# Kernel optimization log

Hardware: AMD Instinct MI355X
Metric: run time of the kernel (lower is better)

The kernel has to match this reference:

```python
import jax, jax.numpy as jnp
import numpy as np

ANCHORS = jnp.array([[10,14],[23,27],[37,58],[81,82],[135,169],[344,319]], jnp.float32)
ANCHOR_MASK = [[3,4,5],[1,2,3]]
NUM_CLASSES = 80
IMAGE_HW = (1080.0, 1920.0)   # (h, w) of source image
MAX_BOXES = 20
SCORE_THR = 0.6
IOU_THR = 0.5
NEG = jnp.float32(-1e30)      # sentinel for suppressed scores


def decode_layer(feats, anchors_l):
    """yolo_head + yolo_correct_boxes for one detection head. feats: [1,H,W,3*(C+5)]."""
    _, H, W, _ = feats.shape
    f = feats.reshape(H, W, 3, NUM_CLASSES + 5)
    gy, gx = jnp.meshgrid(jnp.arange(H), jnp.arange(W), indexing='ij')
    grid = jnp.stack([gx, gy], axis=-1).astype(f.dtype)[:, :, None, :]  # [H,W,1,2] (x,y)
    input_hw = jnp.array([H * 32.0, W * 32.0], f.dtype)                 # network input (h,w)
    # decode
    box_xy = (jax.nn.sigmoid(f[..., :2]) + grid) / jnp.array([W, H], f.dtype)
    box_wh = jnp.exp(f[..., 2:4]) * anchors_l / input_hw[::-1]          # anchors_l: [3,2] (w,h)
    conf = jax.nn.sigmoid(f[..., 4:5])
    probs = jax.nn.sigmoid(f[..., 5:])
    # letterbox correction (yolo_correct_boxes)
    box_yx = box_xy[..., ::-1]
    box_hw = box_wh[..., ::-1]
    image_hw = jnp.array(IMAGE_HW, f.dtype)
    new_shape = jnp.round(image_hw * jnp.min(input_hw / image_hw))
    offset = (input_hw - new_shape) / 2.0 / input_hw
    scale = input_hw / new_shape
    box_yx = (box_yx - offset) * scale
    box_hw = box_hw * scale
    mins = box_yx - box_hw / 2.0
    maxes = box_yx + box_hw / 2.0
    boxes = jnp.concatenate([mins, maxes], axis=-1) * jnp.concatenate([image_hw, image_hw])
    return boxes.reshape(-1, 4), (conf * probs).reshape(-1, NUM_CLASSES)


def nms_per_class(boxes, scores_c):
    """Greedy NMS for one class. boxes: [N,4] (ymin,xmin,ymax,xmax), scores_c: [N].
    Fixed-size (jit-friendly) equivalent of boolean_mask + tf.image.non_max_suppression:
    below-threshold scores are masked to NEG; output is padded to MAX_BOXES slots."""
    areas = (boxes[:, 2] - boxes[:, 0]) * (boxes[:, 3] - boxes[:, 1])
    s0 = jnp.where(scores_c >= SCORE_THR, scores_c, NEG)

    def body(s, _):
        i = jnp.argmax(s)
        valid = s[i] > NEG / 2
        b = boxes[i]
        yx1 = jnp.maximum(b[:2], boxes[:, :2])
        yx2 = jnp.minimum(b[2:], boxes[:, 2:])
        inter = jnp.prod(jnp.clip(yx2 - yx1, 0.0), axis=-1)
        union = areas[i] + areas - inter
        iou = jnp.where(union > 0, inter / union, 0.0)
        s_next = jnp.where((iou > IOU_THR) & valid, NEG, s)
        s_next = s_next.at[i].set(NEG)
        return s_next, (i, valid)

    _, (idx, valid) = jax.lax.scan(body, s0, None, length=MAX_BOXES)
    sel_boxes = boxes[idx] * valid[:, None].astype(boxes.dtype)   # [MAX_BOXES,4]
    sel_scores = scores_c[idx] * valid.astype(scores_c.dtype)     # [MAX_BOXES]
    return sel_boxes, sel_scores, valid


def setup_inputs() -> dict:
    key = jax.random.key(0)
    k0, k1 = jax.random.split(key)
    feats0 = jax.random.normal(k0, (1, 96, 96, 3 * (NUM_CLASSES + 5)), jnp.float32)
    feats1 = jax.random.normal(k1, (1, 192, 192, 3 * (NUM_CLASSES + 5)), jnp.float32)
    return {"feats0": feats0, "feats1": feats1}


def reference(feats0, feats1):
    b0, s0 = decode_layer(feats0, ANCHORS[jnp.array(ANCHOR_MASK[0])])
    b1, s1 = decode_layer(feats1, ANCHORS[jnp.array(ANCHOR_MASK[1])])
    boxes = jnp.concatenate([b0, b1], axis=0)      # [N,4]
    scores = jnp.concatenate([s0, s1], axis=0)     # [N,80]
    sel_b, sel_s, valid = jax.vmap(nms_per_class, in_axes=(None, 1))(boxes, scores)
    classes = jnp.broadcast_to(jnp.arange(NUM_CLASSES, dtype=jnp.int32)[:, None],
                               (NUM_CLASSES, MAX_BOXES))
    classes = jnp.where(valid, classes, -1).reshape(-1)
    return sel_b.reshape(-1, 4), sel_s.reshape(-1), classes
```

## Files before the change

kernel.cpp:

```cpp
#include <hip/hip_runtime.h>

#define NCLS 80
#define MAXB 20
#define N0 27648
#define N1 110592
#define NTOT (N0 + N1)
#define CAP 8192
#define DT 512
#define DSTAGE 3072
#define CNT_STRIDE 16
#define NMS_T 1024
#define NB 256
#define TARGET 128
#define SCAP 256

__device__ __forceinline__ float sigf(float x) {
    return 1.0f / (1.0f + expf(-x));
}

__device__ __forceinline__ unsigned wave_max_bcast(unsigned x) {
    unsigned t;
    t = (unsigned)__builtin_amdgcn_update_dpp((int)x, (int)x, 0x111, 0xF, 0xF, false); x = x > t ? x : t;
    t = (unsigned)__builtin_amdgcn_update_dpp((int)x, (int)x, 0x112, 0xF, 0xF, false); x = x > t ? x : t;
    t = (unsigned)__builtin_amdgcn_update_dpp((int)x, (int)x, 0x114, 0xF, 0xF, false); x = x > t ? x : t;
    t = (unsigned)__builtin_amdgcn_update_dpp((int)x, (int)x, 0x118, 0xF, 0xF, false); x = x > t ? x : t;
    t = (unsigned)__builtin_amdgcn_update_dpp((int)x, (int)x, 0x142, 0xF, 0xF, false); x = x > t ? x : t;
    t = (unsigned)__builtin_amdgcn_update_dpp((int)x, (int)x, 0x143, 0xF, 0xF, false); x = x > t ? x : t;
    return (unsigned)__builtin_amdgcn_readlane((int)x, 63);
}

__device__ __forceinline__ unsigned wave_min_bcast(unsigned x) {
    unsigned t;
    t = (unsigned)__builtin_amdgcn_update_dpp((int)x, (int)x, 0x111, 0xF, 0xF, false); x = x < t ? x : t;
    t = (unsigned)__builtin_amdgcn_update_dpp((int)x, (int)x, 0x112, 0xF, 0xF, false); x = x < t ? x : t;
    t = (unsigned)__builtin_amdgcn_update_dpp((int)x, (int)x, 0x114, 0xF, 0xF, false); x = x < t ? x : t;
    t = (unsigned)__builtin_amdgcn_update_dpp((int)x, (int)x, 0x118, 0xF, 0xF, false); x = x < t ? x : t;
    t = (unsigned)__builtin_amdgcn_update_dpp((int)x, (int)x, 0x142, 0xF, 0xF, false); x = x < t ? x : t;
    t = (unsigned)__builtin_amdgcn_update_dpp((int)x, (int)x, 0x143, 0xF, 0xF, false); x = x < t ? x : t;
    return (unsigned)__builtin_amdgcn_readlane((int)x, 63);
}

__device__ __forceinline__ unsigned wave_incl_scan(unsigned x) {
    x += (unsigned)__builtin_amdgcn_update_dpp(0, (int)x, 0x111, 0xF, 0xF, false);
    x += (unsigned)__builtin_amdgcn_update_dpp(0, (int)x, 0x112, 0xF, 0xF, false);
    x += (unsigned)__builtin_amdgcn_update_dpp(0, (int)x, 0x114, 0xF, 0xF, false);
    x += (unsigned)__builtin_amdgcn_update_dpp(0, (int)x, 0x118, 0xF, 0xF, false);
    x += (unsigned)__builtin_amdgcn_update_dpp(0, (int)x, 0x142, 0xA, 0xF, false);
    x += (unsigned)__builtin_amdgcn_update_dpp(0, (int)x, 0x143, 0xC, 0xF, false);
    return x;
}

__global__ __launch_bounds__(DT) void decode_kernel(
    const float* __restrict__ feats0, const float* __restrict__ feats1,
    float4* __restrict__ boxes, uint2* __restrict__ cands,
    int* __restrict__ counts)
{
    __shared__ unsigned p_gi[DT];
    __shared__ float    p_conf[DT];
    __shared__ int s_npass;
    __shared__ float    s_esc[DSTAGE];
    __shared__ unsigned s_ent[DSTAGE];
    __shared__ int s_n;
    __shared__ int s_cnt[NCLS];
    __shared__ int s_base[NCLS];

    int tid = threadIdx.x;
    if (tid == 0) { s_npass = 0; s_n = 0; }
    for (int c = tid; c < NCLS; c += DT) s_cnt[c] = 0;
    __syncthreads();

    const float* feats;
    int S, base, i;
    float aw0, ah0, aw1, ah1, aw2, ah2;
    if (blockIdx.x < N0 / DT) {
        feats = feats0; S = 96; base = 0;
        i = blockIdx.x * DT + tid;
        aw0 = 81.0f;  ah0 = 82.0f;  aw1 = 135.0f; ah1 = 169.0f; aw2 = 344.0f; ah2 = 319.0f;
    } else {
        feats = feats1; S = 192; base = N0;
        i = (blockIdx.x - N0 / DT) * DT + tid;
        aw0 = 23.0f;  ah0 = 27.0f;  aw1 = 37.0f;  ah1 = 58.0f;  aw2 = 81.0f;  ah2 = 82.0f;
    }

    float sconf = sigf(feats[(size_t)i * 85 + 4]);
    if (sconf >= 0.6f) {
        int sl = atomicAdd(&s_npass, 1);
        p_gi[sl] = (unsigned)(base + i);
        p_conf[sl] = sconf;
    }
    __syncthreads();

    int npass = s_npass;

    for (int e = tid; e < npass; e += DT) {
        int il = (int)p_gi[e] - base;
        int a = il % 3;
        int cell = il / 3;
        int gx = cell % S;
        int gy = cell / S;
        const float* f = feats + (size_t)il * 85;
        float tx = f[0], ty = f[1], tw = f[2], th = f[3];

        float Sf = (float)S;
        float inpf = Sf * 32.0f;
        float aw = (a == 0) ? aw0 : ((a == 1) ? aw1 : aw2);
        float ah = (a == 0) ? ah0 : ((a == 1) ? ah1 : ah2);

        float x = (sigf(tx) + (float)gx) / Sf;
        float y = (sigf(ty) + (float)gy) / Sf;
        float w = expf(tw) * aw / inpf;
        float h = expf(th) * ah / inpf;

        const float OFF = 0.21875f;
        const float SC  = 3072.0f / 1728.0f;
        float yy = (y - OFF) * SC;
        float hh = h * SC;

        boxes[p_gi[e]] = make_float4((yy - hh * 0.5f) * 1080.0f,
                                     (x  - w  * 0.5f) * 1920.0f,
                                     (yy + hh * 0.5f) * 1080.0f,
                                     (x  + w  * 0.5f) * 1920.0f);
    }

    int tot = npass * NCLS;
    for (int wk = tid; wk < tot; wk += DT) {
        int sl = wk / NCLS;
        int c  = wk - sl * NCLS;
        float pv = feats[(size_t)(p_gi[sl] - (unsigned)base) * 85 + 5 + c];
        float s = p_conf[sl] * sigf(pv);
        if (s >= 0.6f) {
            int e = atomicAdd(&s_n, 1);
            if (e < DSTAGE) {
                s_esc[e] = s;
                s_ent[e] = p_gi[sl] | ((unsigned)c << 18);
            }
        }
    }
    __syncthreads();

    int n = s_n < DSTAGE ? s_n : DSTAGE;

    for (int e = tid; e < n; e += DT)
        atomicAdd(&s_cnt[s_ent[e] >> 18], 1);
    __syncthreads();

    for (int c = tid; c < NCLS; c += DT) {
        int k = s_cnt[c];
        s_base[c] = (k > 0) ? atomicAdd(&counts[c * CNT_STRIDE], k) : 0;
        s_cnt[c] = 0;
    }
    __syncthreads();

    for (int e = tid; e < n; e += DT) {
        unsigned ent = s_ent[e];
        int c = ent >> 18;
        int lpos = atomicAdd(&s_cnt[c], 1);
        int pos = s_base[c] + lpos;
        if (pos < CAP)
            cands[(size_t)c * CAP + pos] =
                make_uint2(__float_as_uint(s_esc[e]), ent & 0x3FFFFu);
    }
}

__global__ __launch_bounds__(NMS_T) void nms_kernel(
    const float4* __restrict__ boxes, const uint2* __restrict__ cands,
    const int* __restrict__ counts, float* __restrict__ out)
{
    __shared__ int s_hist[NB];
    __shared__ int s_tau;
    __shared__ int s_m;
    __shared__ float4   s_cbox[SCAP];
    __shared__ unsigned s_csc[SCAP];
    __shared__ unsigned s_cix[SCAP];
    __shared__ unsigned char s_alive[CAP];

    int c = blockIdx.x;
    int tid = threadIdx.x;

    int cnt = counts[c * CNT_STRIDE];
    if (cnt > CAP) cnt = CAP;

    const uint2* cl = cands + (size_t)c * CAP;

    if (tid < NB) s_hist[tid] = 0;
    if (tid == 0) s_m = 0;
    __syncthreads();

    for (int e = tid; e < cnt; e += NMS_T) {
        unsigned sc = cl[e].x;
        atomicAdd(&s_hist[(sc - 0x3F199999u) >> 15], 1);
    }
    __syncthreads();

    if (tid < 64) {
        unsigned acc = 0;
        bool found = false;
        for (int ch = NB / 64 - 1; ch >= 0 && !found; --ch) {
            unsigned h = (unsigned)s_hist[ch * 64 + tid];
            unsigned incl = wave_incl_scan(h);
            unsigned total = (unsigned)__builtin_amdgcn_readlane((int)incl, 63);
            bool ok = acc + (total - incl + h) >= (unsigned)TARGET;
            unsigned long long mk = __ballot(ok);
            if (mk) {
                if (tid == 0) s_tau = ch * 64 + (63 - __builtin_clzll(mk));
                found = true;
            }
            acc += total;
        }
        if (!found && tid == 0) s_tau = 0;
    }
    __syncthreads();

    int tau = s_tau;
    for (int e = tid; e < cnt; e += NMS_T) {
        uint2 v = cl[e];
        if ((int)((v.x - 0x3F199999u) >> 15) >= tau) {
            int p = atomicAdd(&s_m, 1);
            if (p < SCAP) {
                s_csc[p] = v.x;
                s_cix[p] = v.y;
                s_cbox[p] = boxes[v.y];
            }
        }
    }
    __syncthreads();

    if (tid >= 64) return;

    int lane = tid;
    int m = s_m;
    bool need_fb = (m > SCAP);
    if (m > SCAP) m = SCAP;

    float* ob  = out;
    float* os  = out + 6400;
    float* ocl = out + 8000;

    int sel = 0;

    if (!need_fb) {
        unsigned scu[4], ixu[4];
        float4 bx[4];
        float  ar[4];
#pragma unroll
        for (int k = 0; k < 4; ++k) {
            int e = lane + k * 64;
            scu[k] = 0u; ixu[k] = 0xFFFFFFFFu;
            bx[k] = make_float4(0.f, 0.f, 0.f, 0.f);
            ar[k] = 0.f;
            if (e < m) {
                scu[k] = s_csc[e];
                ixu[k] = s_cix[e];
                bx[k] = s_cbox[e];
                ar[k] = (bx[k].z - bx[k].x) * (bx[k].w - bx[k].y);
            }
        }

        for (; sel < MAXB; ++sel) {
            unsigned lm = 0u;
#pragma unroll
            for (int k = 0; k < 4; ++k) lm = lm > scu[k] ? lm : scu[k];
            unsigned smax = wave_max_bcast(lm);
            if (smax == 0u) {
                if (m < cnt) need_fb = true;
                break;
            }
            unsigned li = 0xFFFFFFFFu;
#pragma unroll
            for (int k = 0; k < 4; ++k)
                if (scu[k] == smax && ixu[k] < li) li = ixu[k];
            unsigned bidx = wave_min_bcast(li);

            bool has = false;
            float4 ob_ = make_float4(0.f, 0.f, 0.f, 0.f);
#pragma unroll
            for (int k = 0; k < 4; ++k)
                if (scu[k] == smax && ixu[k] == bidx) { ob_ = bx[k]; has = true; }
            unsigned long long mk = __ballot(has);
            int src = __ffsll((long long)mk) - 1;
            float4 sb;
            sb.x = __int_as_float(__builtin_amdgcn_readlane(__float_as_int(ob_.x), src));
            sb.y = __int_as_float(__builtin_amdgcn_readlane(__float_as_int(ob_.y), src));
            sb.z = __int_as_float(__builtin_amdgcn_readlane(__float_as_int(ob_.z), src));
            sb.w = __int_as_float(__builtin_amdgcn_readlane(__float_as_int(ob_.w), src));
            float area_s = (sb.z - sb.x) * (sb.w - sb.y);

            if (lane == 0) {
                int o = c * MAXB + sel;
                ob[o * 4 + 0] = sb.x; ob[o * 4 + 1] = sb.y;
                ob[o * 4 + 2] = sb.z; ob[o * 4 + 3] = sb.w;
                os[o]  = __uint_as_float(smax);
                ocl[o] = (float)c;
            }

#pragma unroll
            for (int k = 0; k < 4; ++k) {
                if (scu[k] != 0u) {
                    float y1 = fmaxf(sb.x, bx[k].x);
                    float x1 = fmaxf(sb.y, bx[k].y);
                    float y2 = fminf(sb.z, bx[k].z);
                    float x2 = fminf(sb.w, bx[k].w);
                    float inter = fmaxf(y2 - y1, 0.f) * fmaxf(x2 - x1, 0.f);
                    float un = area_s + ar[k] - inter;
                    float iou = (un > 0.f) ? (inter / un) : 0.f;
                    if (iou > 0.5f || ixu[k] == bidx) scu[k] = 0u;
                }
            }
        }
    }

    if (need_fb) {
        for (int e = lane; e < cnt; e += 64) s_alive[e] = 1;
        sel = 0;
        for (; sel < MAXB; ++sel) {
            unsigned bs = 0u, bi = 0xFFFFFFFFu;
            for (int e = lane; e < cnt; e += 64) {
                if (s_alive[e]) {
                    uint2 v = cl[e];
                    if (v.x > bs || (v.x == bs && v.y < bi)) { bs = v.x; bi = v.y; }
                }
            }
            unsigned smax = wave_max_bcast(bs);
            if (smax == 0u) break;
            unsigned li = (bs == smax) ? bi : 0xFFFFFFFFu;
            unsigned bidx = wave_min_bcast(li);

            float4 sb = boxes[bidx];
            float area_s = (sb.z - sb.x) * (sb.w - sb.y);

            if (lane == 0) {
                int o = c * MAXB + sel;
                ob[o * 4 + 0] = sb.x; ob[o * 4 + 1] = sb.y;
                ob[o * 4 + 2] = sb.z; ob[o * 4 + 3] = sb.w;
                os[o]  = __uint_as_float(smax);
                ocl[o] = (float)c;
            }

            for (int e = lane; e < cnt; e += 64) {
                if (s_alive[e]) {
                    uint2 v = cl[e];
                    float4 cb = boxes[v.y];
                    float y1 = fmaxf(sb.x, cb.x);
                    float x1 = fmaxf(sb.y, cb.y);
                    float y2 = fminf(sb.z, cb.z);
                    float x2 = fminf(sb.w, cb.w);
                    float inter = fmaxf(y2 - y1, 0.f) * fmaxf(x2 - x1, 0.f);
                    float area_c = (cb.z - cb.x) * (cb.w - cb.y);
                    float un = area_s + area_c - inter;
                    float iou = (un > 0.f) ? (inter / un) : 0.f;
                    if (iou > 0.5f || v.y == bidx) s_alive[e] = 0;
                }
            }
        }
    }

    for (int q = sel + lane; q < MAXB; q += 64) {
        int o = c * MAXB + q;
        ob[o * 4 + 0] = 0.0f; ob[o * 4 + 1] = 0.0f;
        ob[o * 4 + 2] = 0.0f; ob[o * 4 + 3] = 0.0f;
        os[o]  = 0.0f;
        ocl[o] = -1.0f;
    }
}

extern "C" void kernel_launch(void* const* d_in, const int* in_sizes, int n_in,
                              void* d_out, int out_size, void* d_ws, size_t ws_size,
                              hipStream_t stream) {
    const float* feats0 = (const float*)d_in[0];
    const float* feats1 = (const float*)d_in[1];
    float* out = (float*)d_out;

    char* ws = (char*)d_ws;
    float4* boxes = (float4*)ws;
    int*    counts = (int*)(ws + 2211840);
    uint2*  cands  = (uint2*)(ws + 2211840 + 8192);

    hipMemsetAsync(counts, 0, NCLS * CNT_STRIDE * sizeof(int), stream);

    decode_kernel<<<NTOT / DT, DT, 0, stream>>>(feats0, feats1, boxes, cands, counts);

    nms_kernel<<<NCLS, NMS_T, 0, stream>>>(boxes, cands, counts, out);
}
```

Measured before the change: 51.54 us.

## Fuse memset, decode and NMS into one cooperative kernel with grid syncs

Replaces the memset plus two kernel launches with a single cooperative launch. The counts buffer is cleared in-kernel and separated from decode by a grid.sync, and a second grid.sync separates decode from the per-class NMS, which now runs on the first 80 blocks with 512 threads instead of 1024. Shared memory is unioned between phases to fit the smaller footprint. This removes launch gaps but adds two grid-wide barriers, requires all 270 blocks to be co-resident, and halves the NMS block width.

Result: slower. 113.0 us (+119.3%).

```diff
diff --git a/kernel.cpp b/kernel.cpp
--- a/kernel.cpp
+++ b/kernel.cpp
@@ -1,4 +1,7 @@
 #include <hip/hip_runtime.h>
+#include <hip/hip_cooperative_groups.h>
+
+namespace cg = cooperative_groups;
 
 #define NCLS 80
 #define MAXB 20
@@ -7,9 +10,9 @@
 #define NTOT (N0 + N1)
 #define CAP 8192
 #define DT 512
+#define NBLK (NTOT / DT)
 #define DSTAGE 3072
 #define CNT_STRIDE 16
-#define NMS_T 1024
 #define NB 256
 #define TARGET 128
 #define SCAP 256
@@ -50,35 +53,44 @@
     return x;
 }
 
-__global__ __launch_bounds__(DT) void decode_kernel(
+__global__ __launch_bounds__(DT) void fused_kernel(
     const float* __restrict__ feats0, const float* __restrict__ feats1,
     float4* __restrict__ boxes, uint2* __restrict__ cands,
-    int* __restrict__ counts)
+    int* __restrict__ counts, float* __restrict__ out)
 {
-    __shared__ unsigned p_gi[DT];
-    __shared__ float    p_conf[DT];
-    __shared__ int s_npass;
-    __shared__ float    s_esc[DSTAGE];
-    __shared__ unsigned s_ent[DSTAGE];
-    __shared__ int s_n;
-    __shared__ int s_cnt[NCLS];
-    __shared__ int s_base[NCLS];
+    cg::grid_group grid = cg::this_grid();
+
+    __shared__ __align__(16) char smem[29312];
+    __shared__ int s_npass, s_n, s_tau, s_m;
+
+    unsigned* p_gi   = (unsigned*)(smem);
+    float*    p_conf = (float*)(smem + 2048);
+    float*    s_esc  = (float*)(smem + 4096);
+    unsigned* s_ent  = (unsigned*)(smem + 16384);
+    int*      s_cnt  = (int*)(smem + 28672);
+    int*      s_base = (int*)(smem + 28992);
 
     int tid = threadIdx.x;
+    int blk = blockIdx.x;
+
+    for (int t = blk * DT + tid; t < NCLS * CNT_STRIDE; t += NBLK * DT)
+        counts[t] = 0;
+
     if (tid == 0) { s_npass = 0; s_n = 0; }
     for (int c = tid; c < NCLS; c += DT) s_cnt[c] = 0;
-    __syncthreads();
+
+    grid.sync();
 
     const float* feats;
     int S, base, i;
     float aw0, ah0, aw1, ah1, aw2, ah2;
-    if (blockIdx.x < N0 / DT) {
+    if (blk < N0 / DT) {
         feats = feats0; S = 96; base = 0;
-        i = blockIdx.x * DT + tid;
+        i = blk * DT + tid;
         aw0 = 81.0f;  ah0 = 82.0f;  aw1 = 135.0f; ah1 = 169.0f; aw2 = 344.0f; ah2 = 319.0f;
     } else {
         feats = feats1; S = 192; base = N0;
-        i = (blockIdx.x - N0 / DT) * DT + tid;
+        i = (blk - N0 / DT) * DT + tid;
         aw0 = 23.0f;  ah0 = 27.0f;  aw1 = 37.0f;  ah1 = 58.0f;  aw2 = 81.0f;  ah2 = 82.0f;
     }
 
@@ -160,23 +172,18 @@
             cands[(size_t)c * CAP + pos] =
                 make_uint2(__float_as_uint(s_esc[e]), ent & 0x3FFFFu);
     }
-}
-
-__global__ __launch_bounds__(NMS_T) void nms_kernel(
-    const float4* __restrict__ boxes, const uint2* __restrict__ cands,
-    const int* __restrict__ counts, float* __restrict__ out)
-{
-    __shared__ int s_hist[NB];
-    __shared__ int s_tau;
-    __shared__ int s_m;
-    __shared__ float4   s_cbox[SCAP];
-    __shared__ unsigned s_csc[SCAP];
-    __shared__ unsigned s_cix[SCAP];
-    __shared__ unsigned char s_alive[CAP];
-
-    int c = blockIdx.x;
-    int tid = threadIdx.x;
-
+
+    grid.sync();
+
+    if (blk >= NCLS) return;
+
+    float4*   s_cbox = (float4*)(smem);
+    unsigned* s_csc  = (unsigned*)(smem + 4096);
+    unsigned* s_cix  = (unsigned*)(smem + 5120);
+    int*      s_hist = (int*)(smem + 6144);
+    unsigned char* s_alive = (unsigned char*)(smem + 7168);
+
+    int c = blk;
     int cnt = counts[c * CNT_STRIDE];
     if (cnt > CAP) cnt = CAP;
 
@@ -186,7 +193,7 @@
     if (tid == 0) s_m = 0;
     __syncthreads();
 
-    for (int e = tid; e < cnt; e += NMS_T) {
+    for (int e = tid; e < cnt; e += DT) {
         unsigned sc = cl[e].x;
         atomicAdd(&s_hist[(sc - 0x3F199999u) >> 15], 1);
     }
@@ -212,7 +219,7 @@
     __syncthreads();
 
     int tau = s_tau;
-    for (int e = tid; e < cnt; e += NMS_T) {
+    for (int e = tid; e < cnt; e += DT) {
         uint2 v = cl[e];
         if ((int)((v.x - 0x3F199999u) >> 15) >= tau) {
             int p = atomicAdd(&s_m, 1);
@@ -371,13 +378,12 @@
     float* out = (float*)d_out;
 
     char* ws = (char*)d_ws;
-    float4* boxes = (float4*)ws;
+    float4* boxes  = (float4*)ws;
     int*    counts = (int*)(ws + 2211840);
     uint2*  cands  = (uint2*)(ws + 2211840 + 8192);
 
-    hipMemsetAsync(counts, 0, NCLS * CNT_STRIDE * sizeof(int), stream);
-
-    decode_kernel<<<NTOT / DT, DT, 0, stream>>>(feats0, feats1, boxes, cands, counts);
-
-    nms_kernel<<<NCLS, NMS_T, 0, stream>>>(boxes, cands, counts, out);
-}
+    void* kargs[] = {(void*)&feats0, (void*)&feats1, (void*)&boxes,
+                     (void*)&cands, (void*)&counts, (void*)&out};
+    hipLaunchCooperativeKernel((const void*)fused_kernel, dim3(NBLK), dim3(DT),
+                               kargs, 0, stream);
+}
```
